# Optimization experiments

Measured on AMD Instinct MI355X. Metric: run time of the kernel, lower is better.

The kernel has to match this reference:

```python
import jax, jax.numpy as jnp
import numpy as np

N_NODES = 100000
N_EDGES = 3200000
N_GRAPHS = 512
F_IN = 128
HID = 256
N_LABELS = 10


def setup_inputs() -> dict:
    key = jax.random.key(0)
    ks = jax.random.split(key, 16)
    x = jax.random.normal(ks[0], (N_NODES, F_IN), dtype=jnp.float32)
    edge_index = jax.random.randint(ks[1], (2, N_EDGES), 0, N_NODES)
    batch = jnp.sort(jax.random.randint(ks[2], (N_NODES,), 0, N_GRAPHS))
    dims = [(F_IN, HID), (HID, HID), (HID, HID), (HID, HID // 2), (HID // 2, HID // 2), (HID // 2, HID // 4)]
    inp = {"x": x, "edge_index": edge_index, "batch": batch, "primary_idxs_in_batch": 0}
    for i, (di, do) in enumerate(dims, 1):
        inp[f"W{i}"] = jax.random.normal(ks[2 + i], (di, do), dtype=jnp.float32) * (1.0 / np.sqrt(di))
        inp[f"b{i}"] = jnp.zeros((do,), dtype=jnp.float32)
    inp["Wlin"] = jax.random.normal(ks[12], (HID // 4, N_LABELS), dtype=jnp.float32) * (1.0 / np.sqrt(HID // 4))
    inp["blin"] = jnp.zeros((N_LABELS,), dtype=jnp.float32)
    return inp


def _gcn_conv(h, W, b, src, dst, norm):
    # dense transform first (smaller of the two sides), then normalized scatter-aggregate
    m = (h @ W)[src] * norm[:, None]  # [E+N, C_out]
    return jax.ops.segment_sum(m, dst, num_segments=N_NODES) + b


def reference(x, edge_index, batch, primary_idxs_in_batch,
              W1, b1, W2, b2, W3, b3, W4, b4, W5, b5, W6, b6, Wlin, blin):
    loops = jnp.arange(N_NODES, dtype=edge_index.dtype)
    src = jnp.concatenate([edge_index[0], loops])  # A + I (self loops)
    dst = jnp.concatenate([edge_index[1], loops])
    deg = jax.ops.segment_sum(jnp.ones_like(dst, dtype=x.dtype), dst, num_segments=N_NODES)
    dinv = jnp.where(deg > 0, jax.lax.rsqrt(deg), 0.0)
    norm = dinv[src] * dinv[dst]  # D^-1/2 (A+I) D^-1/2 edge weights

    h = jax.nn.relu(_gcn_conv(x, W1, b1, src, dst, norm))
    h = jax.nn.relu(_gcn_conv(h, W2, b2, src, dst, norm))
    h = jax.nn.relu(_gcn_conv(h, W3, b3, src, dst, norm))
    h = jax.nn.relu(_gcn_conv(h, W4, b4, src, dst, norm))
    h = jax.nn.relu(_gcn_conv(h, W5, b5, src, dst, norm))
    h = _gcn_conv(h, W6, b6, src, dst, norm)

    # primary_idxs_in_batch is falsy (0) -> global_mean_pool path
    s = jax.ops.segment_sum(h, batch, num_segments=N_GRAPHS)
    cnt = jax.ops.segment_sum(jnp.ones((N_NODES,), dtype=h.dtype), batch, num_segments=N_GRAPHS)
    pooled = s / jnp.maximum(cnt, 1.0)[:, None]  # [G, HID//4]

    logits = pooled @ Wlin + blin  # [G, labels]
    return (jax.nn.log_softmax(logits, axis=1), jax.nn.softmax(logits, axis=1))
```

## Files before the change

### kernel.cpp

```cpp
#include <hip/hip_runtime.h>
#include <math.h>

#define NN 100000
#define NE 3200000
#define NG 512
#define NBK 782
#define EBLK 196
#define SBE 16384
#define STSH 13
#define NTIL 13
#define HB 196
#define WB 192
#define QB 12500

typedef __attribute__((ext_vector_type(8))) short short8;
typedef __attribute__((ext_vector_type(4))) float f32x4;
typedef __attribute__((ext_vector_type(2))) float f32x2;

__device__ __forceinline__ float bf2f(unsigned short h){
  return __uint_as_float(((unsigned int)h) << 16);
}
__device__ __forceinline__ unsigned short f2bf(float f){
  unsigned int u = __float_as_uint(f);
  unsigned int r = (u + 0x7fffu + ((u >> 16) & 1u)) >> 16;
  return (unsigned short)r;
}
__device__ __forceinline__ unsigned char f2fp8(float v){
  int p = __builtin_amdgcn_cvt_pk_fp8_f32(v, v, 0, 0);
  return (unsigned char)p;
}

__global__ __launch_bounds__(256) void pre_k(const int* __restrict__ ei,
    int* __restrict__ cnt, int* __restrict__ btot,
    const float* __restrict__ x, unsigned char* __restrict__ xq,
    const float* W1, const float* W2, const float* W3,
    const float* W4, const float* W5, const float* W6,
    unsigned short* O1, unsigned short* O2, unsigned short* O3,
    unsigned short* O4, unsigned short* O5, unsigned short* O6)
{
  __shared__ int lh[NBK];
  int b = blockIdx.x, t = threadIdx.x;
  if (b < HB){
    for (int i=t; i<NBK; i+=256) lh[i] = 0;
    __syncthreads();
    int base = b*SBE;
    #pragma unroll 8
    for (int u=0; u<SBE/256; u++){
      int e = base + u*256 + t;
      if (e < NE) atomicAdd(&lh[ei[NE + e] >> 7], 1);
    }
    __syncthreads();
    for (int i=t; i<NBK; i+=256){
      int v = lh[i];
      cnt[b*NBK + i] = v;
      if (v) atomicAdd(&btot[i], v);
    }
    return;
  }
  if (b < HB + WB){
    int bb = b - HB;
    int cfg = bb >> 5, bx = bb & 31;
    int K, N; const float* W; unsigned short* out;
    switch(cfg){
      case 0: K=128; N=256; W=W1; out=O1; break;
      case 1: K=256; N=256; W=W2; out=O2; break;
      case 2: K=256; N=256; W=W3; out=O3; break;
      case 3: K=256; N=128; W=W4; out=O4; break;
      case 4: K=128; N=128; W=W5; out=O5; break;
      default:K=128; N=64;  W=W6; out=O6; break;
    }
    int idx = bx*256 + t;
    int total = K*N/8;
    if (idx >= total) return;
    int l = idx & 15;
    int tt = idx >> 4; int q = tt & 3; tt >>= 2;
    int NT = N/16;
    int nt = tt % NT, kt = tt / NT;
    int kbase = kt*32 + q*8, n = nt*16 + l;
    short8 o;
    #pragma unroll
    for (int j=0;j<8;j++) o[j] = (short)f2bf(W[(size_t)(kbase+j)*N + n]);
    *(short8*)(out + (size_t)idx*8) = o;
    return;
  }
  {
    int i = (b - HB - WB)*256 + t;
    float4 v = ((const float4*)x)[i];
    int p = __builtin_amdgcn_cvt_pk_fp8_f32(v.x, v.y, 0, 0);
    p = __builtin_amdgcn_cvt_pk_fp8_f32(v.z, v.w, p, 1);
    ((unsigned int*)xq)[i] = (unsigned int)p;
  }
}

__global__ __launch_bounds__(256) void bkpfx_k(int* __restrict__ cnt,
    const int* __restrict__ btot, int* __restrict__ bptr){
  __shared__ int sc[256];
  int b = blockIdx.x, t = threadIdx.x;
  int p = 0;
  for (int i = t; i < b; i += 256) p += btot[i];
  sc[t] = p; __syncthreads();
  for (int off=128; off>0; off>>=1){
    if (t < off) sc[t] += sc[t+off];
    __syncthreads();
  }
  int pb = sc[0];
  __syncthreads();
  if (t == 0){
    bptr[b] = pb;
    if (b == NBK-1) bptr[NBK] = pb + btot[b];
  }
  int v = (t < EBLK) ? cnt[t*NBK + b] : 0;
  sc[t] = v; __syncthreads();
  for (int off=1; off<256; off<<=1){
    int u = (t>=off) ? sc[t-off] : 0;
    __syncthreads(); sc[t] += u; __syncthreads();
  }
  if (t < EBLK) cnt[t*NBK + b] = pb + sc[t] - v;
}
__global__ __launch_bounds__(256) void scat2_k(const int* __restrict__ ei,
    const int* __restrict__ cnt, unsigned int* __restrict__ ebuf){
  __shared__ int lh[NBK];
  __shared__ int lo[NBK];
  int t = threadIdx.x, b = blockIdx.x;
  for (int i=t; i<NBK; i+=256){ lh[i] = 0; lo[i] = cnt[b*NBK + i]; }
  __syncthreads();
  int base = b*SBE;
  #pragma unroll 8
  for (int u=0; u<SBE/256; u++){
    int e = base + u*256 + t;
    if (e < NE){
      int s = ei[e], d = ei[NE + e];
      int bk = d >> 7;
      int r = atomicAdd(&lh[bk], 1);
      ebuf[lo[bk] + r] = (unsigned)s | ((unsigned)(d & 127) << 17);
    }
  }
}
__global__ __launch_bounds__(256) void bcsr_k(const unsigned int* __restrict__ ebuf,
    const int* __restrict__ bptr, int* __restrict__ rp, float* __restrict__ dinv,
    int* __restrict__ col, int* __restrict__ permg){
  __shared__ int cnt2[128*NTIL];
  __shared__ int sc[128];
  __shared__ int dg[128];
  int b = blockIdx.x, t = threadIdx.x;
  int nbase = b << 7;
  int beg = bptr[b], end = bptr[b+1];
  for (int i = t; i < 128*NTIL; i += 256) cnt2[i] = 0;
  __syncthreads();
  for (int e = beg + t; e < end; e += 256){
    unsigned int sd = ebuf[e];
    int li = sd >> 17;
    int tile = (int)(sd & 0x1FFFFu) >> STSH;
    atomicAdd(&cnt2[li*NTIL + tile], 1);
  }
  __syncthreads();
  int v = 0;
  if (t < 128){
    #pragma unroll
    for (int k=0;k<NTIL;k++) v += cnt2[t*NTIL+k];
    sc[t] = v;
    dg[t] = ((nbase + t) < NN) ? v : 0x7FFFFFFF;
  }
  __syncthreads();
  for (int o2=1; o2<128; o2<<=1){
    int u = (t < 128 && t >= o2) ? sc[t-o2] : 0;
    __syncthreads();
    if (t < 128) sc[t] += u;
    __syncthreads();
  }
  if (t < 128){
    int node = nbase + t;
    int ex = beg + sc[t] - v;
    if (node < NN){
      rp[node] = ex;
      dinv[node] = rsqrtf((float)(v + 1));
    }
    int s = ex;
    #pragma unroll
    for (int k=0;k<NTIL;k++){
      int c = cnt2[t*NTIL+k];
      cnt2[t*NTIL+k] = s;
      s += c;
    }
    int d = dg[t];
    int rk = 0;
    #pragma unroll 4
    for (int u2=0; u2<128; u2++){
      int du = dg[u2];
      rk += (int)((du < d) || (du == d && u2 < t));
    }
    permg[nbase + rk] = node;
  }
  if (b == ((NN-1) >> 7) && t == 0) rp[NN] = end;
  __syncthreads();
  for (int e = beg + t; e < end; e += 256){
    unsigned int sd = ebuf[e];
    int li = sd >> 17;
    int src = (int)(sd & 0x1FFFF);
    int tile = src >> STSH;
    int pos = atomicAdd(&cnt2[li*NTIL + tile], 1);
    col[pos] = src;
  }
}

template<int RS, int W, bool SRC_SCALE, bool RELU, bool HAS_BIAS>
__global__ __launch_bounds__(256) void spmm8_k(const unsigned char* __restrict__ in,
    unsigned short* __restrict__ out,
    const int* __restrict__ rp, const int* __restrict__ col,
    const float* __restrict__ dinv, const int* __restrict__ perm,
    const float* __restrict__ bias)
{
  constexpr int LPR = W/16;
  constexpr int RPW = 64/LPR;
  constexpr int GP  = 128/RPW;
  int tid = threadIdx.x;
  int wv = tid >> 6, lane = tid & 63;
  int sub = lane / LPR, li = lane % LPR;
  int G = blockIdx.x*4 + wv;
  int bucket = G % NBK;
  int rg = (GP-1) - (G / NBK);
  int row = perm[(bucket << 7) + rg*RPW + sub];
  if (row >= NN) return;
  int beg = rp[row], end = rp[row+1];
  float di = dinv[row];
  int co = blockIdx.y*W + li*16;
  const unsigned char* inb = in + co;
  f32x2 acc2[8];
  {
    uint4 sv = *(const uint4*)(inb + (size_t)row*RS);
    acc2[0] = __builtin_amdgcn_cvt_pk_f32_fp8(sv.x, 0);
    acc2[1] = __builtin_amdgcn_cvt_pk_f32_fp8(sv.x, 1);
    acc2[2] = __builtin_amdgcn_cvt_pk_f32_fp8(sv.y, 0);
    acc2[3] = __builtin_amdgcn_cvt_pk_f32_fp8(sv.y, 1);
    acc2[4] = __builtin_amdgcn_cvt_pk_f32_fp8(sv.z, 0);
    acc2[5] = __builtin_amdgcn_cvt_pk_f32_fp8(sv.z, 1);
    acc2[6] = __builtin_amdgcn_cvt_pk_f32_fp8(sv.w, 0);
    acc2[7] = __builtin_amdgcn_cvt_pk_f32_fp8(sv.w, 1);
    if (SRC_SCALE){
      f32x2 d2 = (f32x2){di, di};
      #pragma unroll
      for (int k=0;k<8;k++) acc2[k] = acc2[k] * d2;
    }
  }
  int j = beg;
  for (; j+8 <= end; j += 8){
    int s[8]; uint4 v[8]; float wgt[8];
    #pragma unroll
    for (int u=0;u<8;u++) s[u] = col[j+u];
    #pragma unroll
    for (int u=0;u<8;u++) v[u] = *(const uint4*)(inb + (size_t)s[u]*RS);
    if (SRC_SCALE){
      #pragma unroll
      for (int u=0;u<8;u++) wgt[u] = dinv[s[u]];
    }
    #pragma unroll
    for (int u=0;u<8;u++){
      float w = SRC_SCALE ? wgt[u] : 1.f;
      f32x2 w2 = (f32x2){w, w};
      acc2[0] = __builtin_elementwise_fma(w2, __builtin_amdgcn_cvt_pk_f32_fp8(v[u].x, 0), acc2[0]);
      acc2[1] = __builtin_elementwise_fma(w2, __builtin_amdgcn_cvt_pk_f32_fp8(v[u].x, 1), acc2[1]);
      acc2[2] = __builtin_elementwise_fma(w2, __builtin_amdgcn_cvt_pk_f32_fp8(v[u].y, 0), acc2[2]);
      acc2[3] = __builtin_elementwise_fma(w2, __builtin_amdgcn_cvt_pk_f32_fp8(v[u].y, 1), acc2[3]);
      acc2[4] = __builtin_elementwise_fma(w2, __builtin_amdgcn_cvt_pk_f32_fp8(v[u].z, 0), acc2[4]);
      acc2[5] = __builtin_elementwise_fma(w2, __builtin_amdgcn_cvt_pk_f32_fp8(v[u].z, 1), acc2[5]);
      acc2[6] = __builtin_elementwise_fma(w2, __builtin_amdgcn_cvt_pk_f32_fp8(v[u].w, 0), acc2[6]);
      acc2[7] = __builtin_elementwise_fma(w2, __builtin_amdgcn_cvt_pk_f32_fp8(v[u].w, 1), acc2[7]);
    }
  }
  for (; j < end; j++){
    int ss = col[j];
    uint4 v = *(const uint4*)(inb + (size_t)ss*RS);
    float w = SRC_SCALE ? dinv[ss] : 1.f;
    f32x2 w2 = (f32x2){w, w};
    acc2[0] = __builtin_elementwise_fma(w2, __builtin_amdgcn_cvt_pk_f32_fp8(v.x, 0), acc2[0]);
    acc2[1] = __builtin_elementwise_fma(w2, __builtin_amdgcn_cvt_pk_f32_fp8(v.x, 1), acc2[1]);
    acc2[2] = __builtin_elementwise_fma(w2, __builtin_amdgcn_cvt_pk_f32_fp8(v.y, 0), acc2[2]);
    acc2[3] = __builtin_elementwise_fma(w2, __builtin_amdgcn_cvt_pk_f32_fp8(v.y, 1), acc2[3]);
    acc2[4] = __builtin_elementwise_fma(w2, __builtin_amdgcn_cvt_pk_f32_fp8(v.z, 0), acc2[4]);
    acc2[5] = __builtin_elementwise_fma(w2, __builtin_amdgcn_cvt_pk_f32_fp8(v.z, 1), acc2[5]);
    acc2[6] = __builtin_elementwise_fma(w2, __builtin_amdgcn_cvt_pk_f32_fp8(v.w, 0), acc2[6]);
    acc2[7] = __builtin_elementwise_fma(w2, __builtin_amdgcn_cvt_pk_f32_fp8(v.w, 1), acc2[7]);
  }
  float acc[16];
  #pragma unroll
  for (int k=0;k<8;k++){ acc[2*k] = acc2[k][0]; acc[2*k+1] = acc2[k][1]; }
  float bb[16];
  if (HAS_BIAS){
    #pragma unroll
    for (int u=0;u<4;u++) *(float4*)&bb[u*4] = *(const float4*)(bias + co + u*4);
  }
  #pragma unroll
  for (int v=0;v<16;v++){
    acc[v] *= di;
    if (HAS_BIAS) acc[v] += bb[v];
    if (RELU) acc[v] = fmaxf(acc[v], 0.f);
  }
  uint4 o0, o1;
  o0.x = (unsigned int)f2bf(acc[0])  | ((unsigned int)f2bf(acc[1])<<16);
  o0.y = (unsigned int)f2bf(acc[2])  | ((unsigned int)f2bf(acc[3])<<16);
  o0.z = (unsigned int)f2bf(acc[4])  | ((unsigned int)f2bf(acc[5])<<16);
  o0.w = (unsigned int)f2bf(acc[6])  | ((unsigned int)f2bf(acc[7])<<16);
  o1.x = (unsigned int)f2bf(acc[8])  | ((unsigned int)f2bf(acc[9])<<16);
  o1.y = (unsigned int)f2bf(acc[10]) | ((unsigned int)f2bf(acc[11])<<16);
  o1.z = (unsigned int)f2bf(acc[12]) | ((unsigned int)f2bf(acc[13])<<16);
  o1.w = (unsigned int)f2bf(acc[14]) | ((unsigned int)f2bf(acc[15])<<16);
  unsigned short* op = out + (size_t)row*RS + co;
  *(uint4*)op = o0;
  *(uint4*)(op + 8) = o1;
}

template<int K, int N, int EPI>
__global__ __launch_bounds__(256) void mgemm_k(const unsigned short* __restrict__ A,
    const unsigned short* __restrict__ Bsw,
    const float* __restrict__ aux, unsigned short* __restrict__ Cb,
    unsigned char* __restrict__ Cq, int M)
{
  constexpr int NT = 4;
  constexpr int KT = K/32;
  constexpr int NTF = N/16;
  constexpr int NSL = N/64;
  __shared__ short8 Bl[KT*NT*64];
  int tid = threadIdx.x;
  int w = tid >> 6, lane = tid & 63;
  int l = lane & 15, q = lane >> 4;
  int id = blockIdx.x;
  int xcd = id & 7, s = id >> 3;
  int xsl = s % NSL;
  int y = (s / NSL)*8 + xcd;
  if (y >= (M + 255)/256) return;
  int nb0 = xsl * 64;
  int rb = y*256 + w*64;
  {
    const short8* bsrc = (const short8*)Bsw;
    for (int i = tid; i < KT*NT*64; i += 256){
      int kt = i >> 8;
      int rem = i & 255;
      Bl[i] = bsrc[(kt*NTF + (nb0 >> 4))*64 + rem];
    }
  }
  const unsigned short* ap[4];
  #pragma unroll
  for (int rt=0; rt<4; rt++){
    int r = min(rb + rt*16 + l, M-1);
    ap[rt] = A + (size_t)r*K + q*8;
  }
  f32x4 acc[4][NT];
  #pragma unroll
  for (int rt=0; rt<4; rt++)
    #pragma unroll
    for (int nt=0; nt<NT; nt++) acc[rt][nt] = (f32x4){0,0,0,0};
  short8 a[4], an[4];
  #pragma unroll
  for (int rt=0; rt<4; rt++) a[rt] = *(const short8*)(ap[rt]);
  __syncthreads();
  for (int kt=0; kt<KT; kt++){
    if (kt+1 < KT){
      #pragma unroll
      for (int rt=0; rt<4; rt++) an[rt] = *(const short8*)(ap[rt] + (kt+1)*32);
    }
    const short8* bl = &Bl[kt << 8];
    #pragma unroll
    for (int nt=0; nt<NT; nt++){
      short8 bf = bl[nt*64 + q*16 + l];
      acc[0][nt] = __builtin_amdgcn_mfma_f32_16x16x32_bf16(a[0], bf, acc[0][nt], 0,0,0);
      acc[1][nt] = __builtin_amdgcn_mfma_f32_16x16x32_bf16(a[1], bf, acc[1][nt], 0,0,0);
      acc[2][nt] = __builtin_amdgcn_mfma_f32_16x16x32_bf16(a[2], bf, acc[2][nt], 0,0,0);
      acc[3][nt] = __builtin_amdgcn_mfma_f32_16x16x32_bf16(a[3], bf, acc[3][nt], 0,0,0);
    }
    #pragma unroll
    for (int rt=0; rt<4; rt++) a[rt] = an[rt];
  }
  #pragma unroll
  for (int rt=0; rt<4; rt++){
    int rbb = rb + rt*16;
    #pragma unroll
    for (int nt=0; nt<NT; nt++){
      f32x4 av = acc[rt][nt];
      int n = nb0 + nt*16 + l;
      #pragma unroll
      for (int r=0;r<4;r++){
        int row = rbb + q*4 + r;
        if (row < M){
          float v = av[r];
          if (EPI == 0){
            v = fmaxf(v + aux[n], 0.f);
            Cb[(size_t)row*N + n] = f2bf(v);
          } else {
            v *= aux[row];
            Cq[(size_t)row*N + n] = f2fp8(v);
          }
        }
      }
    }
  }
}

__global__ __launch_bounds__(256) void poolhead_k(const unsigned short* __restrict__ h,
    const int* __restrict__ batch, const float* __restrict__ Wlin,
    const float* __restrict__ blin, float* __restrict__ out)
{
  __shared__ int range[2];
  __shared__ float red[4][64];
  __shared__ float pl[64];
  int g = blockIdx.x;
  if (threadIdx.x < 2){
    int target = g + threadIdx.x;
    int lo = 0, hi = NN;
    while (lo < hi){ int m = (lo+hi) >> 1; if (batch[m] < target) lo = m+1; else hi = m; }
    range[threadIdx.x] = lo;
  }
  __syncthreads();
  int lo = range[0], hi = range[1];
  int ch = threadIdx.x & 63, rg = threadIdx.x >> 6;
  float s = 0.f;
  for (int r = lo + rg; r < hi; r += 4) s += bf2f(h[(size_t)r*64 + ch]);
  red[rg][ch] = s; __syncthreads();
  if (rg == 0){
    float tot = red[0][ch] + red[1][ch] + red[2][ch] + red[3][ch];
    pl[ch] = tot / fmaxf((float)(hi - lo), 1.f);
  }
  __syncthreads();
  if (threadIdx.x == 0){
    float l[10];
    #pragma unroll
    for (int j=0;j<10;j++) l[j] = blin[j];
    for (int c=0;c<64;c++){
      float p = pl[c];
      #pragma unroll
      for (int j=0;j<10;j++) l[j] = fmaf(p, Wlin[c*10 + j], l[j]);
    }
    float mx = l[0];
    #pragma unroll
    for (int j=1;j<10;j++) mx = fmaxf(mx, l[j]);
    float e[10]; float se = 0.f;
    #pragma unroll
    for (int j=0;j<10;j++){ e[j] = expf(l[j]-mx); se += e[j]; }
    float lse = logf(se);
    #pragma unroll
    for (int j=0;j<10;j++){
      out[g*10 + j]         = l[j] - mx - lse;
      out[NG*10 + g*10 + j] = e[j] / se;
    }
  }
}

extern "C" void kernel_launch(void* const* d_in, const int* in_sizes, int n_in,
                              void* d_out, int out_size, void* d_ws, size_t ws_size,
                              hipStream_t stream)
{
  const float* x     = (const float*)d_in[0];
  const int*   ei    = (const int*)  d_in[1];
  const int*   batch = (const int*)  d_in[2];
  const float* W1=(const float*)d_in[4],  *b1=(const float*)d_in[5];
  const float* W2=(const float*)d_in[6],  *b2=(const float*)d_in[7];
  const float* W3=(const float*)d_in[8],  *b3=(const float*)d_in[9];
  const float* W4=(const float*)d_in[10], *b4=(const float*)d_in[11];
  const float* W5=(const float*)d_in[12], *b5=(const float*)d_in[13];
  const float* W6=(const float*)d_in[14], *b6=(const float*)d_in[15];
  const float* Wl=(const float*)d_in[16], *bl=(const float*)d_in[17];
  float* out = (float*)d_out;

  char* ws = (char*)d_ws;
  unsigned short* hA  = (unsigned short*)(ws + 0);
  unsigned short* hB  = (unsigned short*)(ws + 51200000);
  unsigned char*  hQ  = (unsigned char*) (ws + 102400000);
  unsigned char*  xq  = (unsigned char*) (ws + 128000000);
  int*   col   = (int*)  (ws + 140800000);
  unsigned int* ebuf = (unsigned int*)(ws + 153600000);
  int*   rp    = (int*)  (ws + 166400000);
  float* dinv  = (float*)(ws + 166800016);
  unsigned short* W1s = (unsigned short*)(ws + 167200016);
  unsigned short* W2s = (unsigned short*)(ws + 167265552);
  unsigned short* W3s = (unsigned short*)(ws + 167396624);
  unsigned short* W4s = (unsigned short*)(ws + 167527696);
  unsigned short* W5s = (unsigned short*)(ws + 167593232);
  unsigned short* W6s = (unsigned short*)(ws + 167626000);
  int*   btot  = (int*)  (ws + 167642896);
  int*   bptr  = (int*)  (ws + 167646032);
  int*   cnt   = (int*)  (ws + 167649184);
  int*   perm  = cnt;

  hipMemsetAsync(btot, 0, NBK*4, stream);

  pre_k <<<HB+WB+QB, 256, 0, stream>>>(ei, cnt, btot, x, xq,
      W1,W2,W3,W4,W5,W6, W1s,W2s,W3s,W4s,W5s,W6s);
  bkpfx_k <<<NBK, 256, 0, stream>>>(cnt, btot, bptr);
  scat2_k <<<EBLK, 256, 0, stream>>>(ei, cnt, ebuf);
  bcsr_k  <<<NBK, 256, 0, stream>>>(ebuf, bptr, rp, dinv, col, perm);

  const int GX128 = NBK*16/4;
  const int GX64  = NBK*8/4;
  const int GT    = (NN + 255)/256;
  const int GY8   = (GT + 7)/8;
  const int G256  = 8*4*GY8;
  const int G128  = 8*2*GY8;
  const int G64   = 8*1*GY8;

  spmm8_k<128,128,true,false,false><<<dim3(GX128,1),256,0,stream>>>(xq, hA, rp, col, dinv, perm, nullptr);
  mgemm_k<128,256,0><<<G256,256,0,stream>>>(hA, W1s, b1, hB, nullptr, NN);
  mgemm_k<256,256,1><<<G256,256,0,stream>>>(hB, W2s, dinv, nullptr, hQ, NN);
  spmm8_k<256,128,false,true,true><<<dim3(GX128,2),256,0,stream>>>(hQ, hA, rp, col, dinv, perm, b2);
  mgemm_k<256,256,1><<<G256,256,0,stream>>>(hA, W3s, dinv, nullptr, hQ, NN);
  spmm8_k<256,128,false,true,true><<<dim3(GX128,2),256,0,stream>>>(hQ, hB, rp, col, dinv, perm, b3);
  mgemm_k<256,128,1><<<G128,256,0,stream>>>(hB, W4s, dinv, nullptr, hQ, NN);
  spmm8_k<128,128,false,true,true><<<dim3(GX128,1),256,0,stream>>>(hQ, hA, rp, col, dinv, perm, b4);
  mgemm_k<128,128,1><<<G128,256,0,stream>>>(hA, W5s, dinv, nullptr, hQ, NN);
  spmm8_k<128,128,false,true,true><<<dim3(GX128,1),256,0,stream>>>(hQ, hB, rp, col, dinv, perm, b5);
  mgemm_k<128,64,1><<<G64,256,0,stream>>>(hB, W6s, dinv, nullptr, hQ, NN);
  spmm8_k<64,64,false,false,true><<<dim3(GX64,1),256,0,stream>>>(hQ, hA, rp, col, dinv, perm, b6);

  poolhead_k<<<NG, 256, 0, stream>>>(hA, batch, Wl, bl, out);
}
```

Before: 962.7 us.

## Shrink GEMM row tile to 64 and stage A rows in swizzled LDS

Each GEMM block now covers 64 rows instead of 256, with each wave handling one 16-row MFMA tile. The A tile is loaded into an XOR-swizzled LDS buffer rather than held as register prefetches. This cuts accumulator registers and quadruples the grid to raise occupancy and parallelism. The cost is that B is loaded into LDS four times as often, each B fragment feeds fewer MFMAs, and the global-to-register prefetch overlap is gone.

```diff
diff --git a/kernel.cpp b/kernel.cpp
--- a/kernel.cpp
+++ b/kernel.cpp
@@ -319,7 +319,9 @@
   constexpr int KT = K/32;
   constexpr int NTF = N/16;
   constexpr int NSL = N/64;
+  constexpr int SEGS = K/8;
   __shared__ short8 Bl[KT*NT*64];
+  __shared__ unsigned char Al[64*K*2];
   int tid = threadIdx.x;
   int w = tid >> 6, lane = tid & 63;
   int l = lane & 15, q = lane >> 4;
@@ -327,9 +329,10 @@
   int xcd = id & 7, s = id >> 3;
   int xsl = s % NSL;
   int y = (s / NSL)*8 + xcd;
-  if (y >= (M + 255)/256) return;
+  int NYT = (M + 63)/64;
+  if (y >= NYT) return;
   int nb0 = xsl * 64;
-  int rb = y*256 + w*64;
+  int rb = y*64;
   {
     const short8* bsrc = (const short8*)Bsw;
     for (int i = tid; i < KT*NT*64; i += 256){
@@ -338,57 +341,46 @@
       Bl[i] = bsrc[(kt*NTF + (nb0 >> 4))*64 + rem];
     }
   }
-  const unsigned short* ap[4];
+  for (int i = tid; i < 64*SEGS; i += 256){
+    int row = i / SEGS, seg = i % SEGS;
+    int gr = rb + row; if (gr >= M) gr = M-1;
+    uint4 v = *(const uint4*)(A + (size_t)gr*K + seg*8);
+    int sw = (seg*16) ^ ((row & 7) << 4);
+    *(uint4*)(&Al[row*(K*2) + sw]) = v;
+  }
+  f32x4 acc[NT];
   #pragma unroll
-  for (int rt=0; rt<4; rt++){
-    int r = min(rb + rt*16 + l, M-1);
-    ap[rt] = A + (size_t)r*K + q*8;
-  }
-  f32x4 acc[4][NT];
-  #pragma unroll
-  for (int rt=0; rt<4; rt++)
-    #pragma unroll
-    for (int nt=0; nt<NT; nt++) acc[rt][nt] = (f32x4){0,0,0,0};
-  short8 a[4], an[4];
-  #pragma unroll
-  for (int rt=0; rt<4; rt++) a[rt] = *(const short8*)(ap[rt]);
-  __syncthreads();
+  for (int nt=0; nt<NT; nt++) acc[nt] = (f32x4){0,0,0,0};
+  __syncthreads();
+  int rowl = w*16 + l;
+  int rbase = rowl*(K*2);
+  int rxor = (rowl & 7) << 4;
   for (int kt=0; kt<KT; kt++){
-    if (kt+1 < KT){
-      #pragma unroll
-      for (int rt=0; rt<4; rt++) an[rt] = *(const short8*)(ap[rt] + (kt+1)*32);
-    }
+    int kb = (kt*32 + q*8)*2;
+    short8 af = *(const short8*)(&Al[rbase + (kb ^ rxor)]);
     const short8* bl = &Bl[kt << 8];
     #pragma unroll
     for (int nt=0; nt<NT; nt++){
       short8 bf = bl[nt*64 + q*16 + l];
-      acc[0][nt] = __builtin_amdgcn_mfma_f32_16x16x32_bf16(a[0], bf, acc[0][nt], 0,0,0);
-      acc[1][nt] = __builtin_amdgcn_mfma_f32_16x16x32_bf16(a[1], bf, acc[1][nt], 0,0,0);
-      acc[2][nt] = __builtin_amdgcn_mfma_f32_16x16x32_bf16(a[2], bf, acc[2][nt], 0,0,0);
-      acc[3][nt] = __builtin_amdgcn_mfma_f32_16x16x32_bf16(a[3], bf, acc[3][nt], 0,0,0);
-    }
-    #pragma unroll
-    for (int rt=0; rt<4; rt++) a[rt] = an[rt];
-  }
+      acc[nt] = __builtin_amdgcn_mfma_f32_16x16x32_bf16(af, bf, acc[nt], 0,0,0);
+    }
+  }
+  int rbb = rb + w*16;
   #pragma unroll
-  for (int rt=0; rt<4; rt++){
-    int rbb = rb + rt*16;
-    #pragma unroll
-    for (int nt=0; nt<NT; nt++){
-      f32x4 av = acc[rt][nt];
-      int n = nb0 + nt*16 + l;
-      #pragma unroll
-      for (int r=0;r<4;r++){
-        int row = rbb + q*4 + r;
-        if (row < M){
-          float v = av[r];
-          if (EPI == 0){
-            v = fmaxf(v + aux[n], 0.f);
-            Cb[(size_t)row*N + n] = f2bf(v);
-          } else {
-            v *= aux[row];
-            Cq[(size_t)row*N + n] = f2fp8(v);
-          }
+  for (int nt=0; nt<NT; nt++){
+    f32x4 av = acc[nt];
+    int n = nb0 + nt*16 + l;
+    #pragma unroll
+    for (int r=0;r<4;r++){
+      int row = rbb + q*4 + r;
+      if (row < M){
+        float v = av[r];
+        if (EPI == 0){
+          v = fmaxf(v + aux[n], 0.f);
+          Cb[(size_t)row*N + n] = f2bf(v);
+        } else {
+          v *= aux[row];
+          Cq[(size_t)row*N + n] = f2fp8(v);
         }
       }
     }
@@ -490,8 +482,8 @@
 
   const int GX128 = NBK*16/4;
   const int GX64  = NBK*8/4;
-  const int GT    = (NN + 255)/256;
-  const int GY8   = (GT + 7)/8;
+  const int NYT   = (NN + 63)/64;
+  const int GY8   = (NYT + 7)/8;
   const int G256  = 8*4*GY8;
   const int G128  = 8*2*GY8;
   const int G64   = 8*1*GY8;
```

Result: no change. 977.3 us (+1.5%).

## Stage A tiles through swizzled double-buffered LDS with 128-row GEMM blocks

Applied to the files above, without the earlier changes.

The dense GEMM kernel now loads 128x64 bf16 A tiles cooperatively with coalesced 16-byte loads into XOR-swizzled, double-buffered shared memory instead of each lane reading strided rows straight from global memory. Row tiles drop from 256 to 128 per block, so each wave handles 32 rows, and the grid doubles. This is meant to improve global-load coalescing and overlap the next tile's load with MFMA work. The cost is more LDS per block (32KB extra), an extra barrier per k-step, and fewer MFMAs per B fragment load, which could lower occupancy or B reuse.

```diff
diff --git a/kernel.cpp b/kernel.cpp
--- a/kernel.cpp
+++ b/kernel.cpp
@@ -319,7 +319,9 @@
   constexpr int KT = K/32;
   constexpr int NTF = N/16;
   constexpr int NSL = N/64;
+  constexpr int NKS = K/64;
   __shared__ short8 Bl[KT*NT*64];
+  __shared__ unsigned char Al[2][128*128];
   int tid = threadIdx.x;
   int w = tid >> 6, lane = tid & 63;
   int l = lane & 15, q = lane >> 4;
@@ -327,9 +329,10 @@
   int xcd = id & 7, s = id >> 3;
   int xsl = s % NSL;
   int y = (s / NSL)*8 + xcd;
-  if (y >= (M + 255)/256) return;
+  int NYT = (M + 127)/128;
+  if (y >= NYT) return;
   int nb0 = xsl * 64;
-  int rb = y*256 + w*64;
+  int rb = y*128;
   {
     const short8* bsrc = (const short8*)Bsw;
     for (int i = tid; i < KT*NT*64; i += 256){
@@ -338,41 +341,55 @@
       Bl[i] = bsrc[(kt*NTF + (nb0 >> 4))*64 + rem];
     }
   }
-  const unsigned short* ap[4];
   #pragma unroll
-  for (int rt=0; rt<4; rt++){
-    int r = min(rb + rt*16 + l, M-1);
-    ap[rt] = A + (size_t)r*K + q*8;
-  }
-  f32x4 acc[4][NT];
+  for (int it = 0; it < 4; it++){
+    int i = it*256 + tid;
+    int row = i >> 3, ch = i & 7;
+    int gr = rb + row; if (gr >= M) gr = M-1;
+    uint4 v = *(const uint4*)(A + (size_t)gr*K + ch*8);
+    *(uint4*)(&Al[0][row*128 + ((ch*16) ^ ((row & 7) << 4))]) = v;
+  }
+  f32x4 acc[2][NT];
   #pragma unroll
-  for (int rt=0; rt<4; rt++)
+  for (int rt=0; rt<2; rt++)
     #pragma unroll
     for (int nt=0; nt<NT; nt++) acc[rt][nt] = (f32x4){0,0,0,0};
-  short8 a[4], an[4];
+  __syncthreads();
+  int buf = 0;
+  for (int ks=0; ks<NKS; ks++){
+    if (ks+1 < NKS){
+      #pragma unroll
+      for (int it = 0; it < 4; it++){
+        int i = it*256 + tid;
+        int row = i >> 3, ch = i & 7;
+        int gr = rb + row; if (gr >= M) gr = M-1;
+        uint4 v = *(const uint4*)(A + (size_t)gr*K + (ks+1)*64 + ch*8);
+        *(uint4*)(&Al[buf^1][row*128 + ((ch*16) ^ ((row & 7) << 4))]) = v;
+      }
+    }
+    #pragma unroll
+    for (int kk=0; kk<2; kk++){
+      int kt = ks*2 + kk;
+      const short8* bl = &Bl[kt << 8];
+      short8 af[2];
+      #pragma unroll
+      for (int rt=0; rt<2; rt++){
+        int row = w*32 + rt*16 + l;
+        af[rt] = *(const short8*)(&Al[buf][row*128 + ((kk*64 + q*16) ^ ((row & 7) << 4))]);
+      }
+      #pragma unroll
+      for (int nt=0; nt<NT; nt++){
+        short8 bf = bl[nt*64 + q*16 + l];
+        acc[0][nt] = __builtin_amdgcn_mfma_f32_16x16x32_bf16(af[0], bf, acc[0][nt], 0,0,0);
+        acc[1][nt] = __builtin_amdgcn_mfma_f32_16x16x32_bf16(af[1], bf, acc[1][nt], 0,0,0);
+      }
+    }
+    __syncthreads();
+    buf ^= 1;
+  }
   #pragma unroll
-  for (int rt=0; rt<4; rt++) a[rt] = *(const short8*)(ap[rt]);
-  __syncthreads();
-  for (int kt=0; kt<KT; kt++){
-    if (kt+1 < KT){
-      #pragma unroll
-      for (int rt=0; rt<4; rt++) an[rt] = *(const short8*)(ap[rt] + (kt+1)*32);
-    }
-    const short8* bl = &Bl[kt << 8];
-    #pragma unroll
-    for (int nt=0; nt<NT; nt++){
-      short8 bf = bl[nt*64 + q*16 + l];
-      acc[0][nt] = __builtin_amdgcn_mfma_f32_16x16x32_bf16(a[0], bf, acc[0][nt], 0,0,0);
-      acc[1][nt] = __builtin_amdgcn_mfma_f32_16x16x32_bf16(a[1], bf, acc[1][nt], 0,0,0);
-      acc[2][nt] = __builtin_amdgcn_mfma_f32_16x16x32_bf16(a[2], bf, acc[2][nt], 0,0,0);
-      acc[3][nt] = __builtin_amdgcn_mfma_f32_16x16x32_bf16(a[3], bf, acc[3][nt], 0,0,0);
-    }
-    #pragma unroll
-    for (int rt=0; rt<4; rt++) a[rt] = an[rt];
-  }
-  #pragma unroll
-  for (int rt=0; rt<4; rt++){
-    int rbb = rb + rt*16;
+  for (int rt=0; rt<2; rt++){
+    int rbb = rb + w*32 + rt*16;
     #pragma unroll
     for (int nt=0; nt<NT; nt++){
       f32x4 av = acc[rt][nt];
@@ -490,8 +507,8 @@
 
   const int GX128 = NBK*16/4;
   const int GX64  = NBK*8/4;
-  const int GT    = (NN + 255)/256;
-  const int GY8   = (GT + 7)/8;
+  const int NYT   = (NN + 127)/128;
+  const int GY8   = (NYT + 7)/8;
   const int G256  = 8*4*GY8;
   const int G128  = 8*2*GY8;
   const int G64   = 8*1*GY8;
```

Result: no change. 957.1 us (-0.6%).
